# Optimization experiments

Hardware: AMD Instinct MI355X
Metric: run time of the kernel (lower is better)

Reference implementation:

```python
import jax, jax.numpy as jnp
import numpy as np

B, T, C = 4, 2048, 1024
N_HEADS = 16
HEAD_DIM = C // N_HEADS


def rotary_embedding(seq_len, dim, dtype=jnp.float32):
    pos = jnp.arange(seq_len, dtype=dtype)[:, None]
    i = jnp.arange(0, dim, 2, dtype=dtype)[None, :]
    theta = pos / jnp.power(10000.0, i / dim)
    return jnp.cos(theta), jnp.sin(theta)


def apply_rotary(x, cos, sin):
    # x: [B, T, H, D]; cos/sin: [T, D//2]
    d = x.shape[-1]
    x1, x2 = x[..., : d // 2], x[..., d // 2 :]
    rotated = jnp.concatenate([-x2, x1], axis=-1)
    cos = jnp.concatenate([cos, cos], axis=-1)[None, :, None, :]
    sin = jnp.concatenate([sin, sin], axis=-1)[None, :, None, :]
    return x * cos + rotated * sin


def setup_inputs() -> dict:
    key = jax.random.key(0)
    k1, k2, k3 = jax.random.split(key, 3)
    x = jax.random.normal(k1, (B, T, C), dtype=jnp.float32)
    # lecun_normal-ish init scale
    w_qkv = jax.random.normal(k2, (C, 3 * C), dtype=jnp.float32) / np.sqrt(C)
    w_out = jax.random.normal(k3, (C, C), dtype=jnp.float32) / np.sqrt(C)
    return {"x": x, "w_qkv": w_qkv, "w_out": w_out}


def reference(x, w_qkv, w_out):
    b, t, c = x.shape
    qkv = jnp.einsum("btc,cd->btd", x, w_qkv)
    q, k, v = jnp.split(qkv, 3, axis=-1)
    q = q.reshape(b, t, N_HEADS, HEAD_DIM)
    k = k.reshape(b, t, N_HEADS, HEAD_DIM)
    v = v.reshape(b, t, N_HEADS, HEAD_DIM)
    cos, sin = rotary_embedding(t, HEAD_DIM, dtype=x.dtype)
    q = apply_rotary(q, cos, sin)
    k = apply_rotary(k, cos, sin)
    scale = jnp.sqrt(jnp.asarray(HEAD_DIM, dtype=x.dtype))
    # scores: [B, H, T, T]
    attn = jnp.einsum("bqhd,bkhd->bhqk", q, k) / scale
    mask = jnp.tril(jnp.ones((t, t), dtype=jnp.bool_))
    attn = jnp.where(mask[None, None, :, :], attn, jnp.asarray(-1e9, dtype=x.dtype))
    attn = jax.nn.softmax(attn, axis=-1)
    out = jnp.einsum("bhqk,bkhd->bqhd", attn, v).reshape(b, t, c)
    return jnp.einsum("btc,cd->btd", out, w_out)
```

## Files before the change

### kernel.cpp

```cpp
#include <hip/hip_runtime.h>
#include <stdint.h>

#define DEVI __device__ __forceinline__

typedef unsigned short ushort_t;
typedef __bf16 bf16x8 __attribute__((ext_vector_type(8)));
typedef float f32x4 __attribute__((ext_vector_type(4)));
typedef unsigned short ushort8 __attribute__((ext_vector_type(8)));
typedef short s16x4 __attribute__((ext_vector_type(4)));

#define BB 4
#define TT 2048
#define CC 1024
#define NH 16
#define HD 64
#define MM (BB*TT)

DEVI ushort_t f2bf(float f) {
    __bf16 h = (__bf16)f;
    return __builtin_bit_cast(ushort_t, h);
}

typedef const __attribute__((address_space(1))) unsigned int guint_t;
typedef __attribute__((address_space(3))) unsigned int luint_t;

DEVI void gl2lds16(const void* g, void* lds) {
    __builtin_amdgcn_global_load_lds((guint_t*)(uintptr_t)g,
                                     (luint_t*)(unsigned int)(uintptr_t)lds,
                                     16, 0, 0);
}

template <int N> DEVI void waitvm() {
    static_assert(N == 0 || N == 6 || N == 8, "unsupported vmcnt literal");
    if constexpr (N == 0)      asm volatile("s_waitcnt vmcnt(0)" ::: "memory");
    else if constexpr (N == 6) asm volatile("s_waitcnt vmcnt(6)" ::: "memory");
    else if constexpr (N == 8) asm volatile("s_waitcnt vmcnt(8)" ::: "memory");
}

__global__ void cvt_f32_bf16(const float* __restrict__ in,
                             ushort_t* __restrict__ out) {
    int i = blockIdx.x * 256 + threadIdx.x;
    const float4* p = (const float4*)in + (size_t)i * 2;
    float4 a = p[0], b = p[1];
    ushort8 r;
    r[0] = f2bf(a.x); r[1] = f2bf(a.y); r[2] = f2bf(a.z); r[3] = f2bf(a.w);
    r[4] = f2bf(b.x); r[5] = f2bf(b.y); r[6] = f2bf(b.z); r[7] = f2bf(b.w);
    *(ushort8*)(out + (size_t)i * 8) = r;
}

__global__ void transpose_f2b(const float* __restrict__ in,
                              ushort_t* __restrict__ out, int R, int Cc) {
    __shared__ ushort_t tile[32][33];
    int bx = blockIdx.x * 32;
    int by = blockIdx.y * 32;
    int tx = threadIdx.x & 31, ty = threadIdx.x >> 5;
    #pragma unroll
    for (int i = 0; i < 4; i++) {
        int r = ty * 4 + i;
        tile[r][tx] = f2bf(in[(size_t)(by + r) * Cc + bx + tx]);
    }
    __syncthreads();
    #pragma unroll
    for (int i = 0; i < 4; i++) {
        int r = ty * 4 + i;
        out[(size_t)(bx + r) * R + by + tx] = tile[tx][r];
    }
}

__global__ void rope_table(float2* __restrict__ tab) {
    int i = blockIdx.x * 256 + threadIdx.x;
    int t = i >> 5, j = i & 31;
    float inv = exp2f((float)j * -0.41524101186092029f);
    float theta = (float)t * inv;
    float s, c;
    sincosf(theta, &s, &c);
    tab[i] = make_float2(c, s);
}

__global__ void vtrans(const ushort_t* __restrict__ Vb,
                       ushort_t* __restrict__ VbT) {
    __shared__ ushort_t tile[64 * 72];
    const int bh = blockIdx.y;
    const int t0 = blockIdx.x * 64;
    const int tid = threadIdx.x;
    const int r = tid >> 2, c = (tid & 3) * 16;
    const size_t base = (size_t)bh * (TT * HD);
    const ushort_t* g = Vb + base + (size_t)(t0 + r) * HD + c;
    *(ushort8*)&tile[r * 72 + c]     = *(const ushort8*)g;
    *(ushort8*)&tile[r * 72 + c + 8] = *(const ushort8*)(g + 8);
    __syncthreads();
    ushort8 a, b;
    #pragma unroll
    for (int j = 0; j < 8; j++) a[j] = tile[(c + j) * 72 + r];
    #pragma unroll
    for (int j = 0; j < 8; j++) b[j] = tile[(c + 8 + j) * 72 + r];
    ushort_t* o = VbT + base + (size_t)r * TT + t0 + c;
    *(ushort8*)o = a;
    *(ushort8*)(o + 8) = b;
}

template <int MODE, int BM>
__global__ __launch_bounds__(512, 2) void gemm_bt(
    const ushort_t* __restrict__ A, const ushort_t* __restrict__ Bt,
    float* __restrict__ CoutF,
    ushort_t* __restrict__ Qb, ushort_t* __restrict__ Kb, ushort_t* __restrict__ Vb,
    const float2* __restrict__ rope, int M, int N, int Kd) {
    constexpr int MR = BM / 32;
    constexpr int AL = BM / 64;
    constexpr int L  = AL + 4;
    constexpr int NK = CC / 64;
    (void)M;

    __shared__ __attribute__((aligned(16))) ushort_t As[2][BM * 64];
    __shared__ __attribute__((aligned(16))) ushort_t Bs[2][256 * 64];

    const int tid = threadIdx.x;
    const int w = tid >> 6, l = tid & 63;
    const int lane15 = l & 15, quad = l >> 4;
    const int wm = (w >> 2) * (BM / 2);
    const int wn = (w & 3) * 64;

    const int nbn = gridDim.x;
    const int nwg = nbn * gridDim.y;
    const int lid = blockIdx.y * nbn + blockIdx.x;
    const int sid = (lid & 7) * (nwg >> 3) + (lid >> 3);
    const int bn = sid % nbn, bm = sid / nbn;

    const int sr8 = l >> 3;
    const int sc  = l & 7;

    auto STAGE = [&](int buf, int k0) {
        #pragma unroll
        for (int i = 0; i < AL; ++i) {
            int r = w * (BM / 8) + i * 8 + sr8;
            int gr = bm * BM + r;
            size_t e;
            if constexpr (MODE == 2)
                e = ((size_t)(gr >> 11)) * 2097152 + ((size_t)(k0 >> 6)) * 131072
                    + (size_t)(gr & (TT - 1)) * 64;
            else
                e = (size_t)gr * Kd + k0;
            const char* g = (const char*)(A + e) + ((sc ^ sr8) * 16);
            gl2lds16(g, (char*)&As[buf][0] + (w * (BM / 8) + i * 8) * 128);
        }
        #pragma unroll
        for (int i = 0; i < 4; ++i) {
            int r = w * 32 + i * 8 + sr8;
            int gr = bn * 256 + r;
            const char* g = (const char*)(Bt + (size_t)gr * Kd + k0)
                            + ((sc ^ sr8) * 16);
            gl2lds16(g, (char*)&Bs[buf][0] + (w * 32 + i * 8) * 128);
        }
    };

    f32x4 acc[MR][4];
    #pragma unroll
    for (int m = 0; m < MR; ++m)
        #pragma unroll
        for (int n = 0; n < 4; ++n)
            acc[m][n] = f32x4{0.f, 0.f, 0.f, 0.f};

    STAGE(0, 0);
    STAGE(1, 64);
    waitvm<L>();
    __builtin_amdgcn_s_barrier();
    asm volatile("" ::: "memory");

    const int swz = (lane15 & 7) << 4;

    for (int k = 0; k < NK; ++k) {
        const char* Asb = (const char*)&As[k & 1][0];
        const char* Bsb = (const char*)&Bs[k & 1][0];
        #pragma unroll
        for (int kk = 0; kk < 2; ++kk) {
            const int cb = (kk * 64 + quad * 16) ^ swz;
            bf16x8 bfr[4];
            #pragma unroll
            for (int n = 0; n < 4; ++n)
                bfr[n] = *(const bf16x8*)(Bsb + (wn + n * 16 + lane15) * 128 + cb);
            bf16x8 af[MR];
            #pragma unroll
            for (int m = 0; m < MR; ++m)
                af[m] = *(const bf16x8*)(Asb + (wm + m * 16 + lane15) * 128 + cb);
            __builtin_amdgcn_s_setprio(1);
            #pragma unroll
            for (int m = 0; m < MR; ++m)
                #pragma unroll
                for (int n = 0; n < 4; ++n)
                    acc[m][n] = __builtin_amdgcn_mfma_f32_16x16x32_bf16(
                        af[m], bfr[n], acc[m][n], 0, 0, 0);
            __builtin_amdgcn_s_setprio(0);
        }
        if (k == NK - 1) break;

        __builtin_amdgcn_sched_barrier(0);
        asm volatile("s_waitcnt lgkmcnt(0)" ::: "memory");
        __builtin_amdgcn_s_barrier();
        asm volatile("" ::: "memory");
        if (k + 2 < NK) { STAGE(k & 1, (k + 2) * 64); waitvm<L>(); }
        else            waitvm<0>();
        __builtin_amdgcn_s_barrier();
        asm volatile("" ::: "memory");
    }

    if constexpr (MODE == 1) {
        const float SCQ = 0.125f * 1.4426950408889634f;
        const int colbase = bn * 256 + wn;
        const int seg = colbase >> 10;
        const int h = (colbase & 1023) >> 6;
        #pragma unroll
        for (int m = 0; m < MR; ++m) {
            int row0 = bm * BM + wm + m * 16 + quad * 4;
            #pragma unroll
            for (int r = 0; r < 4; ++r) {
                int row = row0 + r;
                int b = row >> 11, t = row & (TT - 1);
                size_t ob = ((size_t)(b * NH + h) * TT + t) * HD;
                if (seg == 2) {
                    #pragma unroll
                    for (int n = 0; n < 4; ++n)
                        Vb[ob + n * 16 + lane15] = f2bf(acc[m][n][r]);
                } else {
                    ushort_t* dst = (seg == 0) ? Qb : Kb;
                    #pragma unroll
                    for (int n = 0; n < 2; ++n) {
                        int j = n * 16 + lane15;
                        float2 cs = rope[t * 32 + j];
                        float x1 = acc[m][n][r];
                        float x2 = acc[m][n + 2][r];
                        float y1 = x1 * cs.x - x2 * cs.y;
                        float y2 = x2 * cs.x + x1 * cs.y;
                        if (seg == 0) { y1 *= SCQ; y2 *= SCQ; }
                        dst[ob + j]      = f2bf(y1);
                        dst[ob + 32 + j] = f2bf(y2);
                    }
                }
            }
        }
    } else {
        #pragma unroll
        for (int m = 0; m < MR; ++m) {
            #pragma unroll
            for (int r = 0; r < 4; ++r) {
                size_t rb = (size_t)(bm * BM + wm + m * 16 + quad * 4 + r) * N
                            + bn * 256 + wn;
                #pragma unroll
                for (int n = 0; n < 4; ++n)
                    CoutF[rb + n * 16 + lane15] = acc[m][n][r];
            }
        }
    }
}

__global__ __launch_bounds__(512, 4) void attn_kernel(
    ushort_t* __restrict__ Qb, const ushort_t* __restrict__ Kb,
    const ushort_t* __restrict__ VbT) {
    __shared__ __attribute__((aligned(16))) ushort_t Ks[2][64 * 72];
    __shared__ __attribute__((aligned(16))) ushort_t Vs[2][64 * 72];

    const int tid = threadIdx.x;
    const int w = tid >> 6, l = tid & 63;
    const int lane15 = l & 15, quad = l >> 4;

    const int d = blockIdx.y * gridDim.x + blockIdx.x;
    const int xcd = d & 7, j = d >> 3;
    const int bh = xcd * 8 + (j & 7);
    const int qt = (int)((0x765489AB3210CDEFull >> (4 * (j >> 3))) & 15);
    const size_t base = (size_t)bh * (TT * HD);

    const int sr = tid >> 3;
    const int sd = (tid & 7) * 8;
    const ushort_t* kgb = Kb  + base + (size_t)sr * HD + sd;
    const ushort_t* vgb = VbT + base + (size_t)sr * TT + sd;

    const int q0 = qt * 128;
    const int rbase = q0 + w * 16;
    const int ktmax = 2 * qt + 1;

    bf16x8 qf0, qf1;
    {
        const ushort_t* qp = Qb + base + (size_t)(rbase + lane15) * HD + quad * 8;
        qf0 = *(const bf16x8*)qp;
        qf1 = *(const bf16x8*)(qp + 32);
    }

    f32x4 o[4];
    #pragma unroll
    for (int nt = 0; nt < 4; nt++) o[nt] = f32x4{0.f, 0.f, 0.f, 0.f};
    f32x4 lacc = f32x4{0.f, 0.f, 0.f, 0.f};
    float mrow = -INFINITY;

    const s16x4 ONES = {(short)0x3F80, (short)0x3F80,
                        (short)0x3F80, (short)0x3F80};

    ushort8 kr = *(const ushort8*)kgb;
    ushort8 vr = *(const ushort8*)vgb;
    *(ushort8*)&Ks[0][sr * 72 + sd] = kr;
    *(ushort8*)&Vs[0][sr * 72 + sd] = vr;
    kr = *(const ushort8*)(kgb + (size_t)64 * HD);
    vr = *(const ushort8*)(vgb + 64);
    __syncthreads();

    for (int kt = 0; kt <= ktmax; kt++) {
        const int buf = kt & 1;
        if (kt < ktmax) {
            *(ushort8*)&Ks[buf ^ 1][sr * 72 + sd] = kr;
            *(ushort8*)&Vs[buf ^ 1][sr * 72 + sd] = vr;
        }
        if (kt + 2 <= ktmax) {
            kr = *(const ushort8*)(kgb + (size_t)(kt + 2) * 64 * HD);
            vr = *(const ushort8*)(vgb + (size_t)(kt + 2) * 64);
        }

        if (kt * 64 <= rbase + 15) {
            f32x4 s[4];
            #pragma unroll
            for (int c = 0; c < 4; c++) {
                bf16x8 k0 = *(const bf16x8*)&Ks[buf][(c * 16 + lane15) * 72 + quad * 8];
                bf16x8 k1 = *(const bf16x8*)&Ks[buf][(c * 16 + lane15) * 72 + 32 + quad * 8];
                f32x4 z = f32x4{0.f, 0.f, 0.f, 0.f};
                z = __builtin_amdgcn_mfma_f32_16x16x32_bf16(k0, qf0, z, 0, 0, 0);
                s[c] = __builtin_amdgcn_mfma_f32_16x16x32_bf16(k1, qf1, z, 0, 0, 0);
            }

            const int qrow = rbase + lane15;
            if (kt * 64 + 63 > rbase) {
                #pragma unroll
                for (int c = 0; c < 4; c++)
                    #pragma unroll
                    for (int r = 0; r < 4; r++)
                        if (kt * 64 + c * 16 + quad * 4 + r > qrow) s[c][r] = -1e9f;
            }

            float a0 = fmaxf(fmaxf(s[0][0], s[0][1]), s[0][2]);
            float a1 = fmaxf(fmaxf(s[0][3], s[1][0]), s[1][1]);
            float a2 = fmaxf(fmaxf(s[1][2], s[1][3]), s[2][0]);
            float a3 = fmaxf(fmaxf(s[2][1], s[2][2]), s[2][3]);
            float a4 = fmaxf(fmaxf(s[3][0], s[3][1]), s[3][2]);
            float mt = fmaxf(fmaxf(a0, a1), a2);
            mt = fmaxf(fmaxf(mt, a3), fmaxf(a4, s[3][3]));

            if (!__all(mt - mrow <= 8.0f)) {
                float mf = fmaxf(mt, __shfl_xor(mt, 16, 64));
                mf = fmaxf(mf, __shfl_xor(mf, 32, 64));
                float mn = fmaxf(mrow, mf);
                float alpha = __builtin_amdgcn_exp2f(mrow - mn);
                mrow = mn;
                #pragma unroll
                for (int r = 0; r < 4; r++) {
                    float aO = __shfl(alpha, quad * 4 + r, 64);
                    #pragma unroll
                    for (int nt = 0; nt < 4; nt++) o[nt][r] *= aO;
                    lacc[r] *= aO;
                }
            }

            #pragma unroll
            for (int c = 0; c < 4; c++) {
                s16x4 pf;
                #pragma unroll
                for (int r = 0; r < 4; r++)
                    pf[r] = (short)f2bf(__builtin_amdgcn_exp2f(s[c][r] - mrow));
                lacc = __builtin_amdgcn_mfma_f32_16x16x16bf16_1k(
                    pf, ONES, lacc, 0, 0, 0);
                #pragma unroll
                for (int nt = 0; nt < 4; nt++) {
                    s16x4 vf = *(const s16x4*)&Vs[buf][(nt * 16 + lane15) * 72 +
                                                      c * 16 + quad * 4];
                    o[nt] = __builtin_amdgcn_mfma_f32_16x16x16bf16_1k(
                        pf, vf, o[nt], 0, 0, 0);
                }
            }
        }

        if (kt < ktmax) __syncthreads();
    }

    #pragma unroll
    for (int r = 0; r < 4; r++) {
        float lO = 1.0f / lacc[r];
        size_t rb = base + (size_t)(rbase + quad * 4 + r) * HD;
        #pragma unroll
        for (int nt = 0; nt < 4; nt++)
            Qb[rb + nt * 16 + lane15] = f2bf(o[nt][r] * lO);
    }
}

extern "C" void kernel_launch(void* const* d_in, const int* in_sizes, int n_in,
                              void* d_out, int out_size, void* d_ws, size_t ws_size,
                              hipStream_t stream) {
    const float* x    = (const float*)d_in[0];
    const float* wqkv = (const float*)d_in[1];
    const float* wout = (const float*)d_in[2];
    float* out = (float*)d_out;

    char* ws = (char*)d_ws;
    ushort_t* WqkvT = (ushort_t*)(ws);
    ushort_t* WoutT = (ushort_t*)(ws + 6291456);
    float2*   rope  = (float2*)  (ws + 8388608);
    ushort_t* Xb    = (ushort_t*)(ws + 8912896);
    ushort_t* Qb    = (ushort_t*)(ws + 8912896 + 16777216);
    ushort_t* Kb    = (ushort_t*)(ws + 8912896 + 2 * 16777216);
    ushort_t* Vb    = (ushort_t*)(ws + 8912896 + 3 * 16777216);
    ushort_t* VbT   = Xb;

    cvt_f32_bf16<<<dim3(MM * CC / (256 * 8)), 256, 0, stream>>>(x, Xb);
    transpose_f2b<<<dim3(3 * CC / 32, CC / 32), 256, 0, stream>>>(wqkv, WqkvT, CC, 3 * CC);
    transpose_f2b<<<dim3(CC / 32, CC / 32), 256, 0, stream>>>(wout, WoutT, CC, CC);
    rope_table<<<dim3(256), 256, 0, stream>>>(rope);

    gemm_bt<1, 128><<<dim3(3 * CC / 256, MM / 128), 512, 0, stream>>>(
        Xb, WqkvT, nullptr, Qb, Kb, Vb, rope, MM, 3 * CC, CC);

    vtrans<<<dim3(TT / 64, BB * NH), 256, 0, stream>>>(Vb, VbT);

    attn_kernel<<<dim3(16, BB * NH), 512, 0, stream>>>(Qb, Kb, VbT);

    gemm_bt<2, 128><<<dim3(CC / 256, MM / 128), 512, 0, stream>>>(
        Qb, WoutT, out, nullptr, nullptr, nullptr, nullptr, MM, CC, CC);
}
```

Measured before the change: 264.4 us.

## Restructure GEMM main loop into quadrant-interleaved MFMA with staggered LDS prefetch

Rewrites the bf16 GEMM inner loop so each K-tile is processed as four 32x32 MFMA quadrants per wave, with LDS fragment loads and global-to-LDS prefetches of the next tiles interleaved between quadrants under barriers. The aim is to hide global load latency and LDS reads behind MFMA work, where before each tile was computed in one block and then followed by a bulk restage and wait. It adds many more workgroup barriers per iteration and fixes the tile to BM=128. The staging-buffer reuse pattern is intricate, so ordering mistakes could cause races.

Measured after the change: 275.6 us. +4.2%, slower.

```diff
diff --git a/kernel.cpp b/kernel.cpp
--- a/kernel.cpp
+++ b/kernel.cpp
@@ -31,11 +31,15 @@
 }
 
 template <int N> DEVI void waitvm() {
-    static_assert(N == 0 || N == 6 || N == 8, "unsupported vmcnt literal");
+    static_assert(N == 0 || N == 6, "unsupported vmcnt literal");
     if constexpr (N == 0)      asm volatile("s_waitcnt vmcnt(0)" ::: "memory");
     else if constexpr (N == 6) asm volatile("s_waitcnt vmcnt(6)" ::: "memory");
-    else if constexpr (N == 8) asm volatile("s_waitcnt vmcnt(8)" ::: "memory");
-}
+}
+
+#define BARF() do { asm volatile("" ::: "memory"); \
+                    __builtin_amdgcn_s_barrier(); \
+                    asm volatile("" ::: "memory"); } while (0)
+#define LGK0() asm volatile("s_waitcnt lgkmcnt(0)" ::: "memory")
 
 __global__ void cvt_f32_bf16(const float* __restrict__ in,
                              ushort_t* __restrict__ out) {
@@ -99,25 +103,22 @@
     *(ushort8*)(o + 8) = b;
 }
 
-template <int MODE, int BM>
+template <int MODE>
 __global__ __launch_bounds__(512, 2) void gemm_bt(
     const ushort_t* __restrict__ A, const ushort_t* __restrict__ Bt,
     float* __restrict__ CoutF,
     ushort_t* __restrict__ Qb, ushort_t* __restrict__ Kb, ushort_t* __restrict__ Vb,
     const float2* __restrict__ rope, int M, int N, int Kd) {
-    constexpr int MR = BM / 32;
-    constexpr int AL = BM / 64;
-    constexpr int L  = AL + 4;
     constexpr int NK = CC / 64;
     (void)M;
 
-    __shared__ __attribute__((aligned(16))) ushort_t As[2][BM * 64];
+    __shared__ __attribute__((aligned(16))) ushort_t As[2][128 * 64];
     __shared__ __attribute__((aligned(16))) ushort_t Bs[2][256 * 64];
 
     const int tid = threadIdx.x;
     const int w = tid >> 6, l = tid & 63;
     const int lane15 = l & 15, quad = l >> 4;
-    const int wm = (w >> 2) * (BM / 2);
+    const int wm = (w >> 2) * 64;
     const int wn = (w & 3) * 64;
 
     const int nbn = gridDim.x;
@@ -126,82 +127,103 @@
     const int sid = (lid & 7) * (nwg >> 3) + (lid >> 3);
     const int bn = sid % nbn, bm = sid / nbn;
 
-    const int sr8 = l >> 3;
-    const int sc  = l & 7;
-
-    auto STAGE = [&](int buf, int k0) {
-        #pragma unroll
-        for (int i = 0; i < AL; ++i) {
-            int r = w * (BM / 8) + i * 8 + sr8;
-            int gr = bm * BM + r;
-            size_t e;
-            if constexpr (MODE == 2)
-                e = ((size_t)(gr >> 11)) * 2097152 + ((size_t)(k0 >> 6)) * 131072
-                    + (size_t)(gr & (TT - 1)) * 64;
-            else
-                e = (size_t)gr * Kd + k0;
-            const char* g = (const char*)(A + e) + ((sc ^ sr8) * 16);
-            gl2lds16(g, (char*)&As[buf][0] + (w * (BM / 8) + i * 8) * 128);
-        }
-        #pragma unroll
-        for (int i = 0; i < 4; ++i) {
-            int r = w * 32 + i * 8 + sr8;
-            int gr = bn * 256 + r;
-            const char* g = (const char*)(Bt + (size_t)gr * Kd + k0)
-                            + ((sc ^ sr8) * 16);
-            gl2lds16(g, (char*)&Bs[buf][0] + (w * 32 + i * 8) * 128);
-        }
+    const int sr = tid >> 3;
+    const int sc = tid & 7;
+    const int srcswz = (sc ^ (sr & 7)) * 16;
+
+    auto stA = [&](int buf, int t, int ln) {
+        int gr = bm * 128 + ln * 64 + sr;
+        size_t e;
+        if constexpr (MODE == 2)
+            e = (size_t)(gr >> 11) * 2097152 + (size_t)t * 131072
+                + (size_t)(gr & (TT - 1)) * 64;
+        else
+            e = (size_t)gr * (size_t)Kd + (size_t)t * 64;
+        gl2lds16((const char*)(A + e) + srcswz,
+                 (char*)&As[buf][0] + ln * 8192 + tid * 16);
     };
-
-    f32x4 acc[MR][4];
-    #pragma unroll
-    for (int m = 0; m < MR; ++m)
+    auto stB = [&](int buf, int t, int ln) {
+        int gr = bn * 256 + ln * 64 + sr;
+        size_t e = (size_t)gr * (size_t)Kd + (size_t)t * 64;
+        gl2lds16((const char*)(Bt + e) + srcswz,
+                 (char*)&Bs[buf][0] + ln * 8192 + tid * 16);
+    };
+
+    f32x4 acc[4][4];
+    #pragma unroll
+    for (int m = 0; m < 4; ++m)
         #pragma unroll
         for (int n = 0; n < 4; ++n)
             acc[m][n] = f32x4{0.f, 0.f, 0.f, 0.f};
 
-    STAGE(0, 0);
-    STAGE(1, 64);
-    waitvm<L>();
-    __builtin_amdgcn_s_barrier();
-    asm volatile("" ::: "memory");
+    stA(0, 0, 0); stA(0, 0, 1);
+    stB(0, 0, 0); stB(0, 0, 1); stB(0, 0, 2); stB(0, 0, 3);
+    waitvm<0>();
+    BARF();
 
     const int swz = (lane15 & 7) << 4;
-
-    for (int k = 0; k < NK; ++k) {
-        const char* Asb = (const char*)&As[k & 1][0];
-        const char* Bsb = (const char*)&Bs[k & 1][0];
-        #pragma unroll
-        for (int kk = 0; kk < 2; ++kk) {
-            const int cb = (kk * 64 + quad * 16) ^ swz;
-            bf16x8 bfr[4];
-            #pragma unroll
-            for (int n = 0; n < 4; ++n)
-                bfr[n] = *(const bf16x8*)(Bsb + (wn + n * 16 + lane15) * 128 + cb);
-            bf16x8 af[MR];
-            #pragma unroll
-            for (int m = 0; m < MR; ++m)
-                af[m] = *(const bf16x8*)(Asb + (wm + m * 16 + lane15) * 128 + cb);
-            __builtin_amdgcn_s_setprio(1);
-            #pragma unroll
-            for (int m = 0; m < MR; ++m)
-                #pragma unroll
-                for (int n = 0; n < 4; ++n)
-                    acc[m][n] = __builtin_amdgcn_mfma_f32_16x16x32_bf16(
-                        af[m], bfr[n], acc[m][n], 0, 0, 0);
-            __builtin_amdgcn_s_setprio(0);
-        }
-        if (k == NK - 1) break;
-
-        __builtin_amdgcn_sched_barrier(0);
-        asm volatile("s_waitcnt lgkmcnt(0)" ::: "memory");
-        __builtin_amdgcn_s_barrier();
-        asm volatile("" ::: "memory");
-        if (k + 2 < NK) { STAGE(k & 1, (k + 2) * 64); waitvm<L>(); }
-        else            waitvm<0>();
-        __builtin_amdgcn_s_barrier();
-        asm volatile("" ::: "memory");
-    }
+    bf16x8 aR[2][2];
+    bf16x8 bR[2][2][2];
+
+#define LDA_SET(P, MH)                                                        \
+    { _Pragma("unroll") for (int i = 0; i < 2; ++i)                           \
+      _Pragma("unroll") for (int kk = 0; kk < 2; ++kk)                        \
+        aR[i][kk] = *(const bf16x8*)((const char*)&As[P][0] +                 \
+            (wm + MH * 32 + i * 16 + lane15) * 128 +                          \
+            ((kk * 64 + quad * 16) ^ swz)); }
+
+#define LDB_SET(P, NH)                                                        \
+    { _Pragma("unroll") for (int j = 0; j < 2; ++j)                           \
+      _Pragma("unroll") for (int kk = 0; kk < 2; ++kk)                        \
+        bR[NH][j][kk] = *(const bf16x8*)((const char*)&Bs[P][0] +             \
+            (wn + (NH * 2 + j) * 16 + lane15) * 128 +                         \
+            ((kk * 64 + quad * 16) ^ swz)); }
+
+#define MFMA_Q(MH, NH)                                                        \
+    { __builtin_amdgcn_s_setprio(1);                                          \
+      _Pragma("unroll") for (int kk = 0; kk < 2; ++kk)                        \
+      _Pragma("unroll") for (int i = 0; i < 2; ++i)                           \
+      _Pragma("unroll") for (int j = 0; j < 2; ++j)                           \
+        acc[MH * 2 + i][NH * 2 + j] =                                         \
+            __builtin_amdgcn_mfma_f32_16x16x32_bf16(                          \
+                aR[i][kk], bR[NH][j][kk], acc[MH * 2 + i][NH * 2 + j],        \
+                0, 0, 0);                                                     \
+      __builtin_amdgcn_s_setprio(0); }
+
+    for (int t = 0; t < NK; ++t) {
+        const int p = t & 1;
+        const bool st1 = (t + 1 < NK);
+        LDA_SET(p, 0);
+        LDB_SET(p, 0);
+        if (st1) { stA(p ^ 1, t + 1, 0); stA(p ^ 1, t + 1, 1); }
+        BARF(); LGK0();
+        MFMA_Q(0, 0);
+        BARF();
+        LDB_SET(p, 1);
+        if (st1) { stB(p ^ 1, t + 1, 0); stB(p ^ 1, t + 1, 1); }
+        BARF(); LGK0();
+        MFMA_Q(0, 1);
+        BARF();
+        LDA_SET(p, 1);
+        if (st1) { stB(p ^ 1, t + 1, 2); stB(p ^ 1, t + 1, 3); }
+        BARF(); LGK0();
+        MFMA_Q(1, 1);
+        BARF();
+        if (t + 2 < NK) {
+            stA(p, t + 2, 0); stA(p, t + 2, 1);
+            stB(p, t + 2, 0); stB(p, t + 2, 1);
+            stB(p, t + 2, 2); stB(p, t + 2, 3);
+        }
+        MFMA_Q(1, 0);
+        if (st1) {
+            if (t + 2 < NK) waitvm<6>();
+            else            waitvm<0>();
+            BARF();
+        }
+    }
+#undef LDA_SET
+#undef LDB_SET
+#undef MFMA_Q
 
     if constexpr (MODE == 1) {
         const float SCQ = 0.125f * 1.4426950408889634f;
@@ -209,8 +231,8 @@
         const int seg = colbase >> 10;
         const int h = (colbase & 1023) >> 6;
         #pragma unroll
-        for (int m = 0; m < MR; ++m) {
-            int row0 = bm * BM + wm + m * 16 + quad * 4;
+        for (int m = 0; m < 4; ++m) {
+            int row0 = bm * 128 + wm + m * 16 + quad * 4;
             #pragma unroll
             for (int r = 0; r < 4; ++r) {
                 int row = row0 + r;
@@ -239,10 +261,10 @@
         }
     } else {
         #pragma unroll
-        for (int m = 0; m < MR; ++m) {
+        for (int m = 0; m < 4; ++m) {
             #pragma unroll
             for (int r = 0; r < 4; ++r) {
-                size_t rb = (size_t)(bm * BM + wm + m * 16 + quad * 4 + r) * N
+                size_t rb = (size_t)(bm * 128 + wm + m * 16 + quad * 4 + r) * N
                             + bn * 256 + wn;
                 #pragma unroll
                 for (int n = 0; n < 4; ++n)
@@ -409,13 +431,13 @@
     transpose_f2b<<<dim3(CC / 32, CC / 32), 256, 0, stream>>>(wout, WoutT, CC, CC);
     rope_table<<<dim3(256), 256, 0, stream>>>(rope);
 
-    gemm_bt<1, 128><<<dim3(3 * CC / 256, MM / 128), 512, 0, stream>>>(
+    gemm_bt<1><<<dim3(3 * CC / 256, MM / 128), 512, 0, stream>>>(
         Xb, WqkvT, nullptr, Qb, Kb, Vb, rope, MM, 3 * CC, CC);
 
     vtrans<<<dim3(TT / 64, BB * NH), 256, 0, stream>>>(Vb, VbT);
 
     attn_kernel<<<dim3(16, BB * NH), 512, 0, stream>>>(Qb, Kb, VbT);
 
-    gemm_bt<2, 128><<<dim3(CC / 256, MM / 128), 512, 0, stream>>>(
+    gemm_bt<2><<<dim3(CC / 256, MM / 128), 512, 0, stream>>>(
         Qb, WoutT, out, nullptr, nullptr, nullptr, nullptr, MM, CC, CC);
 }
```
